# Optimization experiments

Hardware: AMD Instinct MI355X
Metric: run time of the kernel (lower is better)

Reference implementation:

```python
import jax, jax.numpy as jnp
import numpy as np

N_NODES = 50000


def _sage_conv(x, src, dst, W_l, b_l, W_r):
    # mean aggregation of source-node features at destination nodes
    msg_sum = jax.ops.segment_sum(x[src], dst, num_segments=N_NODES)  # [N, d_in]
    deg = jax.ops.segment_sum(jnp.ones((src.shape[0],), x.dtype), dst,
                              num_segments=N_NODES)  # [N]
    mean = msg_sum / jnp.maximum(deg, 1.0)[:, None]
    # SAGEConv: lin_l(aggr) + lin_r(x); lin_l has bias, lin_r does not
    return mean @ W_l + b_l + x @ W_r


def setup_inputs() -> dict:
    key = jax.random.key(0)
    ks = jax.random.split(key, 8)
    d_in, d_hid, d_out = 128, 128, 64
    E = 800000
    s = lambda k, shp: jax.random.normal(k, shp, dtype=jnp.float32) * (1.0 / np.sqrt(shp[0]))
    return {
        "x": jax.random.normal(ks[0], (N_NODES, d_in), dtype=jnp.float32),
        "edge_index": jax.random.randint(ks[1], (2, E), 0, N_NODES, dtype=jnp.int64
                                         if jax.config.jax_enable_x64 else jnp.int32),
        "W_l1": s(ks[2], (d_in, d_hid)),
        "b_l1": jnp.zeros((d_hid,), jnp.float32),
        "W_r1": s(ks[3], (d_in, d_hid)),
        "W_l2": s(ks[4], (d_hid, d_out)),
        "b_l2": jnp.zeros((d_out,), jnp.float32),
        "W_r2": s(ks[5], (d_hid, d_out)),
    }


def reference(x, edge_index, W_l1, b_l1, W_r1, W_l2, b_l2, W_r2):
    src, dst = edge_index[0], edge_index[1]
    h = _sage_conv(x, src, dst, W_l1, b_l1, W_r1)
    h = jax.nn.relu(h)  # dropout is identity in eval mode
    h = _sage_conv(h, src, dst, W_l2, b_l2, W_r2)
    return h
```

## Files before the change

### kernel.cpp

```cpp
#include <hip/hip_runtime.h>
#include <hip/hip_bf16.h>

#define N_NODES 50000
#define M_TILES 3125
#define NBUCKET 196
#define CAP 5120
#define CHUNK_A 3125
#define CONV_BLOCKS 6250

typedef __attribute__((ext_vector_type(8))) __bf16 bf16x8;
typedef __attribute__((ext_vector_type(4))) float f32x4;

#define OFF_OFF   0
#define OFFE_OFF  200192
#define EBUF_OFF  400384
#define GCUR_OFF  2407424
#define INV_OFF   3800576
#define XBF_OFF   4000768
#define AGG_OFF   16800768
#define PAIRS_OFF 29600768
#define PBF_OFF   42400768
#define WP1_OFF   48800768
#define WP2_OFF   48866304

__device__ __forceinline__ unsigned bfbits(float f) {
    unsigned u = __float_as_uint(f);
    return (u + 0x7fffu + ((u >> 16) & 1u)) & 0xffff0000u;
}
__device__ __forceinline__ unsigned short bf16r(float f) {
    return (unsigned short)(bfbits(f) >> 16);
}
__device__ __forceinline__ float blo(unsigned u) { return __uint_as_float(u << 16); }
__device__ __forceinline__ float bhi(unsigned u) { return __uint_as_float(u & 0xffff0000u); }

__global__ __launch_bounds__(256) void prep_kernel(const float4* __restrict__ x4,
                                                   uint2* __restrict__ xbf,
                                                   int* __restrict__ gcur,
                                                   const float* __restrict__ Wl1,
                                                   const float* __restrict__ Wr1,
                                                   const float* __restrict__ Wl2,
                                                   const float* __restrict__ Wr2,
                                                   unsigned short* __restrict__ Wp1,
                                                   unsigned short* __restrict__ Wp2) {
    int bid = blockIdx.x;
    int t = threadIdx.x;
    if (bid < CONV_BLOCKS) {
        if (bid == 0 && t < NBUCKET) gcur[t] = 0;
        int i = bid * 256 + t;
        float4 v = x4[i];
        uint2 o;
        o.x = (bfbits(v.x) >> 16) | bfbits(v.y);
        o.y = (bfbits(v.z) >> 16) | bfbits(v.w);
        xbf[i] = o;
    } else if (bid < CONV_BLOCKS + 128) {
        int idx = (bid - CONV_BLOCKS) * 256 + t;
        int k = idx >> 7, n = idx & 127;
        float v = (k < 128) ? Wl1[k * 128 + n] : Wr1[(k - 128) * 128 + n];
        Wp1[((k >> 5) << 12) + (n << 5) + (((k >> 3) & 3) << 3) + (k & 7)] = bf16r(v);
    } else {
        int idx = (bid - CONV_BLOCKS - 128) * 256 + t;
        int k = idx >> 7, n = idx & 127;
        float v = (n < 64) ? Wl2[k * 64 + n] : Wr2[k * 64 + (n - 64)];
        Wp2[((k >> 5) << 12) + (n << 5) + (((k >> 3) & 3) << 3) + (k & 7)] = bf16r(v);
    }
}

__global__ __launch_bounds__(256) void passA_kernel(const int* __restrict__ src,
                                                    const int* __restrict__ dst,
                                                    int* __restrict__ gcur,
                                                    unsigned* __restrict__ pairs, int E) {
    __shared__ int bh[256];
    __shared__ int lcur[256];
    __shared__ int gb[256];
    __shared__ int sc[256];
    __shared__ unsigned lbuf[3328];
    int t = threadIdx.x;
    int e0 = blockIdx.x * CHUNK_A;
    int e1 = min(e0 + CHUNK_A, E);
    bh[t] = 0;
    lcur[t] = 0;
    __syncthreads();
    for (int e = e0 + t; e < e1; e += 256) atomicAdd(&bh[dst[e] >> 8], 1);
    __syncthreads();
    int v = bh[t];
    sc[t] = v;
    __syncthreads();
    for (int d = 1; d < 256; d <<= 1) {
        int u = (t >= d) ? sc[t - d] : 0;
        __syncthreads();
        sc[t] += u;
        __syncthreads();
    }
    int lbase = sc[t] - v;
    if (v > 0) gb[t] = t * CAP + atomicAdd(&gcur[t], v);
    bh[t] = lbase;
    __syncthreads();
    for (int e = e0 + t; e < e1; e += 256) {
        int s = src[e], d = dst[e];
        int b = d >> 8;
        int lpos = bh[b] + atomicAdd(&lcur[b], 1);
        lbuf[lpos] = (unsigned)s | ((unsigned)d << 16);
    }
    __syncthreads();
    int T = e1 - e0;
    for (int k = t; k < T; k += 256) {
        unsigned p = lbuf[k];
        int b = p >> 24;
        pairs[gb[b] + (k - bh[b])] = p;
    }
}

__global__ __launch_bounds__(256) void passB_kernel(const int* __restrict__ gcur,
                                                    const unsigned* __restrict__ pairs,
                                                    int* __restrict__ off,
                                                    int* __restrict__ offE,
                                                    float* __restrict__ invdeg,
                                                    unsigned short* __restrict__ ebuf16) {
    __shared__ int sc[256];
    __shared__ int fh[256];
    __shared__ int lcnt[256];
    __shared__ unsigned short lout[CAP];
    int b = blockIdx.x;
    int t = threadIdx.x;
    int gb = b * CAP;
    int W = gcur[b];
    fh[t] = 0;
    __syncthreads();
    for (int k = t; k < W; k += 256) atomicAdd(&fh[(pairs[gb + k] >> 16) & 255], 1);
    __syncthreads();
    int c = fh[t];
    sc[t] = c;
    __syncthreads();
    for (int d = 1; d < 256; d <<= 1) {
        int u = (t >= d) ? sc[t - d] : 0;
        __syncthreads();
        sc[t] += u;
        __syncthreads();
    }
    int excl = sc[t] - c;
    int dg = b * 256 + t;
    if (dg < N_NODES) {
        off[dg] = gb + excl;
        offE[dg] = gb + excl + c;
        invdeg[dg] = 1.0f / fmaxf((float)c, 1.0f);
    }
    lcnt[t] = excl;
    __syncthreads();
    for (int k = t; k < W; k += 256) {
        unsigned p = pairs[gb + k];
        int dl = (p >> 16) & 255;
        int pos = atomicAdd(&lcnt[dl], 1);
        lout[pos] = (unsigned short)(p & 0xffffu);
    }
    __syncthreads();
    for (int k = t; k < W; k += 256) ebuf16[gb + k] = lout[k];
}

__global__ __launch_bounds__(64) void gather1_kernel(const int* __restrict__ off,
                                                     const int* __restrict__ offE,
                                                     const unsigned short* __restrict__ ebuf,
                                                     const float* __restrict__ invdeg,
                                                     const uint4* __restrict__ xbf4,
                                                     uint4* __restrict__ aggbf4) {
    int d = blockIdx.x;
    int j = threadIdx.x;
    int g = j >> 4;
    int f = j & 15;
    int lo = off[d], hi = offE[d];
    float a[8] = {0.f, 0.f, 0.f, 0.f, 0.f, 0.f, 0.f, 0.f};
    int i = lo + g;
    for (; i + 12 < hi; i += 16) {
        int s0 = ebuf[i], s1 = ebuf[i + 4], s2 = ebuf[i + 8], s3 = ebuf[i + 12];
        uint4 v0 = xbf4[(size_t)s0 * 16 + f];
        uint4 v1 = xbf4[(size_t)s1 * 16 + f];
        uint4 v2 = xbf4[(size_t)s2 * 16 + f];
        uint4 v3 = xbf4[(size_t)s3 * 16 + f];
        a[0] += blo(v0.x) + blo(v1.x) + blo(v2.x) + blo(v3.x);
        a[1] += bhi(v0.x) + bhi(v1.x) + bhi(v2.x) + bhi(v3.x);
        a[2] += blo(v0.y) + blo(v1.y) + blo(v2.y) + blo(v3.y);
        a[3] += bhi(v0.y) + bhi(v1.y) + bhi(v2.y) + bhi(v3.y);
        a[4] += blo(v0.z) + blo(v1.z) + blo(v2.z) + blo(v3.z);
        a[5] += bhi(v0.z) + bhi(v1.z) + bhi(v2.z) + bhi(v3.z);
        a[6] += blo(v0.w) + blo(v1.w) + blo(v2.w) + blo(v3.w);
        a[7] += bhi(v0.w) + bhi(v1.w) + bhi(v2.w) + bhi(v3.w);
    }
    for (; i < hi; i += 4) {
        uint4 v = xbf4[(size_t)ebuf[i] * 16 + f];
        a[0] += blo(v.x); a[1] += bhi(v.x);
        a[2] += blo(v.y); a[3] += bhi(v.y);
        a[4] += blo(v.z); a[5] += bhi(v.z);
        a[6] += blo(v.w); a[7] += bhi(v.w);
    }
#pragma unroll
    for (int q = 0; q < 8; ++q) {
        a[q] += __shfl_xor(a[q], 16, 64);
        a[q] += __shfl_xor(a[q], 32, 64);
    }
    if (g == 0) {
        float inv = invdeg[d];
        uint4 o;
        o.x = (bfbits(a[0] * inv) >> 16) | bfbits(a[1] * inv);
        o.y = (bfbits(a[2] * inv) >> 16) | bfbits(a[3] * inv);
        o.z = (bfbits(a[4] * inv) >> 16) | bfbits(a[5] * inv);
        o.w = (bfbits(a[6] * inv) >> 16) | bfbits(a[7] * inv);
        aggbf4[(size_t)d * 16 + f] = o;
    }
}

__global__ __launch_bounds__(256) void gemmF_kernel(const unsigned short* __restrict__ aggbf,
                                                    const unsigned short* __restrict__ xbf,
                                                    const unsigned short* __restrict__ Wp1,
                                                    const float* __restrict__ b1,
                                                    const unsigned short* __restrict__ Wp2,
                                                    const float* __restrict__ b2,
                                                    unsigned short* __restrict__ pbf,
                                                    float* __restrict__ out) {
    __shared__ unsigned short hsm[4][2][2048];
    int w = threadIdx.x >> 6;
    int pairIdx = blockIdx.x * 4 + w;
    int tile0 = pairIdx * 2;
    int tile1 = tile0 + 1;
    bool act0 = tile0 < M_TILES;
    bool act1 = tile1 < M_TILES;
    int t0 = act0 ? tile0 : 0;
    int t1 = act1 ? tile1 : 0;
    int lane = threadIdx.x & 63;
    int lo16 = lane & 15;
    int kg = lane >> 4;
    int r0 = kg * 4;

    f32x4 accA[8], accB[8];
#pragma unroll
    for (int n = 0; n < 8; ++n) {
        accA[n] = (f32x4){0.f, 0.f, 0.f, 0.f};
        accB[n] = (f32x4){0.f, 0.f, 0.f, 0.f};
    }
    const unsigned short* rowa0 = aggbf + (size_t)(t0 * 16 + lo16) * 128;
    const unsigned short* rowx0 = xbf + (size_t)(t0 * 16 + lo16) * 128;
    const unsigned short* rowa1 = aggbf + (size_t)(t1 * 16 + lo16) * 128;
    const unsigned short* rowx1 = xbf + (size_t)(t1 * 16 + lo16) * 128;
#pragma unroll
    for (int ks = 0; ks < 8; ++ks) {
        int ao = (ks < 4 ? ks * 32 : (ks - 4) * 32) + kg * 8;
        bf16x8 a0 = *reinterpret_cast<const bf16x8*>((ks < 4 ? rowa0 : rowx0) + ao);
        bf16x8 a1 = *reinterpret_cast<const bf16x8*>((ks < 4 ? rowa1 : rowx1) + ao);
        const unsigned short* wbase = Wp1 + ks * 4096 + lo16 * 32 + kg * 8;
#pragma unroll
        for (int n = 0; n < 8; ++n) {
            bf16x8 b = *reinterpret_cast<const bf16x8*>(wbase + n * 512);
            accA[n] = __builtin_amdgcn_mfma_f32_16x16x32_bf16(a0, b, accA[n], 0, 0, 0);
            accB[n] = __builtin_amdgcn_mfma_f32_16x16x32_bf16(a1, b, accB[n], 0, 0, 0);
        }
    }

    unsigned short* hs0 = hsm[w][0];
    unsigned short* hs1 = hsm[w][1];
#pragma unroll
    for (int n = 0; n < 8; ++n) {
        int col = n * 16 + lo16;
        float bv = b1[col];
#pragma unroll
        for (int r = 0; r < 4; ++r) {
            int row = r0 + r;
            int sw = (col ^ ((row & 7) << 3));
            hs0[row * 128 + sw] = bf16r(fmaxf(accA[n][r] + bv, 0.0f));
            hs1[row * 128 + sw] = bf16r(fmaxf(accB[n][r] + bv, 0.0f));
        }
    }
    __syncthreads();

    f32x4 acc2A[8], acc2B[8];
#pragma unroll
    for (int n = 0; n < 8; ++n) {
        acc2A[n] = (f32x4){0.f, 0.f, 0.f, 0.f};
        acc2B[n] = (f32x4){0.f, 0.f, 0.f, 0.f};
    }
#pragma unroll
    for (int ks = 0; ks < 4; ++ks) {
        int base0 = (ks * 32 + kg * 8) ^ ((lo16 & 7) << 3);
        bf16x8 a20 = *reinterpret_cast<const bf16x8*>(&hs0[lo16 * 128 + base0]);
        bf16x8 a21 = *reinterpret_cast<const bf16x8*>(&hs1[lo16 * 128 + base0]);
        const unsigned short* wbase = Wp2 + ks * 4096 + lo16 * 32 + kg * 8;
#pragma unroll
        for (int n = 0; n < 8; ++n) {
            bf16x8 b = *reinterpret_cast<const bf16x8*>(wbase + n * 512);
            acc2A[n] = __builtin_amdgcn_mfma_f32_16x16x32_bf16(a20, b, acc2A[n], 0, 0, 0);
            acc2B[n] = __builtin_amdgcn_mfma_f32_16x16x32_bf16(a21, b, acc2B[n], 0, 0, 0);
        }
    }

#pragma unroll
    for (int n = 0; n < 8; ++n) {
        int col = n * 16 + lo16;
        if (col < 64) {
#pragma unroll
            for (int r = 0; r < 4; ++r) {
                if (act0) pbf[(size_t)(tile0 * 16 + r0 + r) * 64 + col] = bf16r(acc2A[n][r]);
                if (act1) pbf[(size_t)(tile1 * 16 + r0 + r) * 64 + col] = bf16r(acc2B[n][r]);
            }
        } else {
            float bv = b2[col - 64];
#pragma unroll
            for (int r = 0; r < 4; ++r) {
                if (act0) out[(size_t)(tile0 * 16 + r0 + r) * 64 + (col - 64)] = acc2A[n][r] + bv;
                if (act1) out[(size_t)(tile1 * 16 + r0 + r) * 64 + (col - 64)] = acc2B[n][r] + bv;
            }
        }
    }
}

__global__ __launch_bounds__(64) void gather2_kernel(const int* __restrict__ off,
                                                     const int* __restrict__ offE,
                                                     const unsigned short* __restrict__ ebuf,
                                                     const float* __restrict__ invdeg,
                                                     const uint2* __restrict__ pbf2,
                                                     float4* __restrict__ out4) {
    int d = blockIdx.x;
    int j = threadIdx.x;
    int g = j >> 4;
    int f = j & 15;
    int lo = off[d], hi = offE[d];
    float a0 = 0.f, a1 = 0.f, a2 = 0.f, a3 = 0.f;
    int i = lo + g;
    for (; i + 12 < hi; i += 16) {
        int s0 = ebuf[i], s1 = ebuf[i + 4], s2 = ebuf[i + 8], s3 = ebuf[i + 12];
        uint2 v0 = pbf2[(size_t)s0 * 16 + f];
        uint2 v1 = pbf2[(size_t)s1 * 16 + f];
        uint2 v2 = pbf2[(size_t)s2 * 16 + f];
        uint2 v3 = pbf2[(size_t)s3 * 16 + f];
        a0 += blo(v0.x) + blo(v1.x) + blo(v2.x) + blo(v3.x);
        a1 += bhi(v0.x) + bhi(v1.x) + bhi(v2.x) + bhi(v3.x);
        a2 += blo(v0.y) + blo(v1.y) + blo(v2.y) + blo(v3.y);
        a3 += bhi(v0.y) + bhi(v1.y) + bhi(v2.y) + bhi(v3.y);
    }
    for (; i < hi; i += 4) {
        uint2 v = pbf2[(size_t)ebuf[i] * 16 + f];
        a0 += blo(v.x); a1 += bhi(v.x);
        a2 += blo(v.y); a3 += bhi(v.y);
    }
    a0 += __shfl_xor(a0, 16, 64); a0 += __shfl_xor(a0, 32, 64);
    a1 += __shfl_xor(a1, 16, 64); a1 += __shfl_xor(a1, 32, 64);
    a2 += __shfl_xor(a2, 16, 64); a2 += __shfl_xor(a2, 32, 64);
    a3 += __shfl_xor(a3, 16, 64); a3 += __shfl_xor(a3, 32, 64);
    if (g == 0) {
        float inv = invdeg[d];
        float4* op = out4 + (size_t)d * 16 + f;
        float4 o = *op;
        o.x += a0 * inv;
        o.y += a1 * inv;
        o.z += a2 * inv;
        o.w += a3 * inv;
        *op = o;
    }
}

extern "C" void kernel_launch(void* const* d_in, const int* in_sizes, int n_in,
                              void* d_out, int out_size, void* d_ws, size_t ws_size,
                              hipStream_t stream) {
    const float* x   = (const float*)d_in[0];
    const int*   ei  = (const int*)d_in[1];
    const float* Wl1 = (const float*)d_in[2];
    const float* b1  = (const float*)d_in[3];
    const float* Wr1 = (const float*)d_in[4];
    const float* Wl2 = (const float*)d_in[5];
    const float* b2  = (const float*)d_in[6];
    const float* Wr2 = (const float*)d_in[7];
    float* out = (float*)d_out;

    const int E = in_sizes[1] / 2;
    const int* src = ei;
    const int* dst = ei + E;

    char* ws = (char*)d_ws;
    int*            off    = (int*)(ws + OFF_OFF);
    int*            offE   = (int*)(ws + OFFE_OFF);
    unsigned short* ebuf16 = (unsigned short*)(ws + EBUF_OFF);
    int*            gcur   = (int*)(ws + GCUR_OFF);
    float*          invdeg = (float*)(ws + INV_OFF);
    unsigned*       xbf    = (unsigned*)(ws + XBF_OFF);
    unsigned*       aggbf  = (unsigned*)(ws + AGG_OFF);
    unsigned*       pairs  = (unsigned*)(ws + PAIRS_OFF);
    unsigned short* pbf    = (unsigned short*)(ws + PBF_OFF);
    unsigned short* Wp1    = (unsigned short*)(ws + WP1_OFF);
    unsigned short* Wp2    = (unsigned short*)(ws + WP2_OFF);

    prep_kernel<<<CONV_BLOCKS + 192, 256, 0, stream>>>((const float4*)x, (uint2*)xbf, gcur,
                                                       Wl1, Wr1, Wl2, Wr2, Wp1, Wp2);

    passA_kernel<<<(E + CHUNK_A - 1) / CHUNK_A, 256, 0, stream>>>(src, dst, gcur, pairs, E);
    passB_kernel<<<NBUCKET, 256, 0, stream>>>(gcur, pairs, off, offE, invdeg, ebuf16);

    gather1_kernel<<<N_NODES, 64, 0, stream>>>(off, offE, ebuf16, invdeg, (const uint4*)xbf,
                                               (uint4*)aggbf);

    gemmF_kernel<<<(((M_TILES + 1) / 2) + 3) / 4, 256, 0, stream>>>(
        (const unsigned short*)aggbf, (const unsigned short*)xbf,
        Wp1, b1, Wp2, b2, pbf, out);

    gather2_kernel<<<N_NODES, 64, 0, stream>>>(off, offE, ebuf16, invdeg, (const uint2*)pbf,
                                               (float4*)out);
}
```

Baseline: 112.4 us.

## Fuse layer-1 gather into GEMM kernel and merge prep with bucketing pass

The first-layer neighbour gather is folded into the fused GEMM kernel. Each wave aggregates its own 16-node tile, with 4 lanes per node, into swizzled LDS, so the bf16 aggregate buffer is no longer written to and read back from global memory. The conversion/prep kernel and passA are merged into one launch, and gcur is zeroed with a memset. The cost is a less parallel gather: one wave per 16 nodes, serial over edges per lane with many registers, which may reduce memory-level parallelism and occupancy compared with the per-node 64-thread gather. GEMM tile pairing per wave is also dropped.

```diff
diff --git a/kernel.cpp b/kernel.cpp
--- a/kernel.cpp
+++ b/kernel.cpp
@@ -17,7 +17,6 @@
 #define GCUR_OFF  2407424
 #define INV_OFF   3800576
 #define XBF_OFF   4000768
-#define AGG_OFF   16800768
 #define PAIRS_OFF 29600768
 #define PBF_OFF   42400768
 #define WP1_OFF   48800768
@@ -33,39 +32,15 @@
 __device__ __forceinline__ float blo(unsigned u) { return __uint_as_float(u << 16); }
 __device__ __forceinline__ float bhi(unsigned u) { return __uint_as_float(u & 0xffff0000u); }
 
-__global__ __launch_bounds__(256) void prep_kernel(const float4* __restrict__ x4,
-                                                   uint2* __restrict__ xbf,
-                                                   int* __restrict__ gcur,
-                                                   const float* __restrict__ Wl1,
-                                                   const float* __restrict__ Wr1,
-                                                   const float* __restrict__ Wl2,
-                                                   const float* __restrict__ Wr2,
-                                                   unsigned short* __restrict__ Wp1,
-                                                   unsigned short* __restrict__ Wp2) {
-    int bid = blockIdx.x;
-    int t = threadIdx.x;
-    if (bid < CONV_BLOCKS) {
-        if (bid == 0 && t < NBUCKET) gcur[t] = 0;
-        int i = bid * 256 + t;
-        float4 v = x4[i];
-        uint2 o;
-        o.x = (bfbits(v.x) >> 16) | bfbits(v.y);
-        o.y = (bfbits(v.z) >> 16) | bfbits(v.w);
-        xbf[i] = o;
-    } else if (bid < CONV_BLOCKS + 128) {
-        int idx = (bid - CONV_BLOCKS) * 256 + t;
-        int k = idx >> 7, n = idx & 127;
-        float v = (k < 128) ? Wl1[k * 128 + n] : Wr1[(k - 128) * 128 + n];
-        Wp1[((k >> 5) << 12) + (n << 5) + (((k >> 3) & 3) << 3) + (k & 7)] = bf16r(v);
-    } else {
-        int idx = (bid - CONV_BLOCKS - 128) * 256 + t;
-        int k = idx >> 7, n = idx & 127;
-        float v = (n < 64) ? Wl2[k * 64 + n] : Wr2[k * 64 + (n - 64)];
-        Wp2[((k >> 5) << 12) + (n << 5) + (((k >> 3) & 3) << 3) + (k & 7)] = bf16r(v);
-    }
-}
-
-__global__ __launch_bounds__(256) void passA_kernel(const int* __restrict__ src,
+__global__ __launch_bounds__(256) void prepA_kernel(const float4* __restrict__ x4,
+                                                    uint2* __restrict__ xbf,
+                                                    const float* __restrict__ Wl1,
+                                                    const float* __restrict__ Wr1,
+                                                    const float* __restrict__ Wl2,
+                                                    const float* __restrict__ Wr2,
+                                                    unsigned short* __restrict__ Wp1,
+                                                    unsigned short* __restrict__ Wp2,
+                                                    const int* __restrict__ src,
                                                     const int* __restrict__ dst,
                                                     int* __restrict__ gcur,
                                                     unsigned* __restrict__ pairs, int E) {
@@ -74,8 +49,35 @@
     __shared__ int gb[256];
     __shared__ int sc[256];
     __shared__ unsigned lbuf[3328];
+    int bid = blockIdx.x;
     int t = threadIdx.x;
-    int e0 = blockIdx.x * CHUNK_A;
+    if (bid < CONV_BLOCKS) {
+        int i = bid * 256 + t;
+        float4 v = x4[i];
+        uint2 o;
+        o.x = (bfbits(v.x) >> 16) | bfbits(v.y);
+        o.y = (bfbits(v.z) >> 16) | bfbits(v.w);
+        xbf[i] = o;
+        return;
+    }
+    bid -= CONV_BLOCKS;
+    if (bid < 128) {
+        int idx = bid * 256 + t;
+        int k = idx >> 7, n = idx & 127;
+        float v = (k < 128) ? Wl1[k * 128 + n] : Wr1[(k - 128) * 128 + n];
+        Wp1[((k >> 5) << 12) + (n << 5) + (((k >> 3) & 3) << 3) + (k & 7)] = bf16r(v);
+        return;
+    }
+    bid -= 128;
+    if (bid < 64) {
+        int idx = bid * 256 + t;
+        int k = idx >> 7, n = idx & 127;
+        float v = (n < 64) ? Wl2[k * 64 + n] : Wr2[k * 64 + (n - 64)];
+        Wp2[((k >> 5) << 12) + (n << 5) + (((k >> 3) & 3) << 3) + (k & 7)] = bf16r(v);
+        return;
+    }
+    bid -= 64;
+    int e0 = bid * CHUNK_A;
     int e1 = min(e0 + CHUNK_A, E);
     bh[t] = 0;
     lcur[t] = 0;
@@ -156,58 +158,11 @@
     for (int k = t; k < W; k += 256) ebuf16[gb + k] = lout[k];
 }
 
-__global__ __launch_bounds__(64) void gather1_kernel(const int* __restrict__ off,
-                                                     const int* __restrict__ offE,
-                                                     const unsigned short* __restrict__ ebuf,
-                                                     const float* __restrict__ invdeg,
-                                                     const uint4* __restrict__ xbf4,
-                                                     uint4* __restrict__ aggbf4) {
-    int d = blockIdx.x;
-    int j = threadIdx.x;
-    int g = j >> 4;
-    int f = j & 15;
-    int lo = off[d], hi = offE[d];
-    float a[8] = {0.f, 0.f, 0.f, 0.f, 0.f, 0.f, 0.f, 0.f};
-    int i = lo + g;
-    for (; i + 12 < hi; i += 16) {
-        int s0 = ebuf[i], s1 = ebuf[i + 4], s2 = ebuf[i + 8], s3 = ebuf[i + 12];
-        uint4 v0 = xbf4[(size_t)s0 * 16 + f];
-        uint4 v1 = xbf4[(size_t)s1 * 16 + f];
-        uint4 v2 = xbf4[(size_t)s2 * 16 + f];
-        uint4 v3 = xbf4[(size_t)s3 * 16 + f];
-        a[0] += blo(v0.x) + blo(v1.x) + blo(v2.x) + blo(v3.x);
-        a[1] += bhi(v0.x) + bhi(v1.x) + bhi(v2.x) + bhi(v3.x);
-        a[2] += blo(v0.y) + blo(v1.y) + blo(v2.y) + blo(v3.y);
-        a[3] += bhi(v0.y) + bhi(v1.y) + bhi(v2.y) + bhi(v3.y);
-        a[4] += blo(v0.z) + blo(v1.z) + blo(v2.z) + blo(v3.z);
-        a[5] += bhi(v0.z) + bhi(v1.z) + bhi(v2.z) + bhi(v3.z);
-        a[6] += blo(v0.w) + blo(v1.w) + blo(v2.w) + blo(v3.w);
-        a[7] += bhi(v0.w) + bhi(v1.w) + bhi(v2.w) + bhi(v3.w);
-    }
-    for (; i < hi; i += 4) {
-        uint4 v = xbf4[(size_t)ebuf[i] * 16 + f];
-        a[0] += blo(v.x); a[1] += bhi(v.x);
-        a[2] += blo(v.y); a[3] += bhi(v.y);
-        a[4] += blo(v.z); a[5] += bhi(v.z);
-        a[6] += blo(v.w); a[7] += bhi(v.w);
-    }
-#pragma unroll
-    for (int q = 0; q < 8; ++q) {
-        a[q] += __shfl_xor(a[q], 16, 64);
-        a[q] += __shfl_xor(a[q], 32, 64);
-    }
-    if (g == 0) {
-        float inv = invdeg[d];
-        uint4 o;
-        o.x = (bfbits(a[0] * inv) >> 16) | bfbits(a[1] * inv);
-        o.y = (bfbits(a[2] * inv) >> 16) | bfbits(a[3] * inv);
-        o.z = (bfbits(a[4] * inv) >> 16) | bfbits(a[5] * inv);
-        o.w = (bfbits(a[6] * inv) >> 16) | bfbits(a[7] * inv);
-        aggbf4[(size_t)d * 16 + f] = o;
-    }
-}
-
-__global__ __launch_bounds__(256) void gemmF_kernel(const unsigned short* __restrict__ aggbf,
+__global__ __launch_bounds__(256) void fuse1_kernel(const int* __restrict__ off,
+                                                    const int* __restrict__ offE,
+                                                    const unsigned short* __restrict__ ebuf,
+                                                    const float* __restrict__ invdeg,
+                                                    const uint4* __restrict__ xbf4,
                                                     const unsigned short* __restrict__ xbf,
                                                     const unsigned short* __restrict__ Wp1,
                                                     const float* __restrict__ b1,
@@ -215,46 +170,88 @@
                                                     const float* __restrict__ b2,
                                                     unsigned short* __restrict__ pbf,
                                                     float* __restrict__ out) {
-    __shared__ unsigned short hsm[4][2][2048];
+    __shared__ unsigned short lsm[4][2048];
     int w = threadIdx.x >> 6;
-    int pairIdx = blockIdx.x * 4 + w;
-    int tile0 = pairIdx * 2;
-    int tile1 = tile0 + 1;
-    bool act0 = tile0 < M_TILES;
-    bool act1 = tile1 < M_TILES;
-    int t0 = act0 ? tile0 : 0;
-    int t1 = act1 ? tile1 : 0;
+    int tile = blockIdx.x * 4 + w;
+    if (tile >= M_TILES) return;
     int lane = threadIdx.x & 63;
+    unsigned short* ls = lsm[w];
+
+    int node = tile * 16 + (lane >> 2);
+    int q = lane & 3;
+    int lo = off[node], hi = offE[node];
+    float a[4][8];
+#pragma unroll
+    for (int u = 0; u < 4; ++u)
+#pragma unroll
+        for (int j = 0; j < 8; ++j) a[u][j] = 0.f;
+    int i = lo;
+    for (; i + 1 < hi; i += 2) {
+        int s0 = ebuf[i], s1 = ebuf[i + 1];
+        uint4 v0[4], v1[4];
+#pragma unroll
+        for (int u = 0; u < 4; ++u) v0[u] = xbf4[(size_t)s0 * 16 + q * 4 + u];
+#pragma unroll
+        for (int u = 0; u < 4; ++u) v1[u] = xbf4[(size_t)s1 * 16 + q * 4 + u];
+#pragma unroll
+        for (int u = 0; u < 4; ++u) {
+            a[u][0] += blo(v0[u].x) + blo(v1[u].x); a[u][1] += bhi(v0[u].x) + bhi(v1[u].x);
+            a[u][2] += blo(v0[u].y) + blo(v1[u].y); a[u][3] += bhi(v0[u].y) + bhi(v1[u].y);
+            a[u][4] += blo(v0[u].z) + blo(v1[u].z); a[u][5] += bhi(v0[u].z) + bhi(v1[u].z);
+            a[u][6] += blo(v0[u].w) + blo(v1[u].w); a[u][7] += bhi(v0[u].w) + bhi(v1[u].w);
+        }
+    }
+    if (i < hi) {
+        int s0 = ebuf[i];
+#pragma unroll
+        for (int u = 0; u < 4; ++u) {
+            uint4 v = xbf4[(size_t)s0 * 16 + q * 4 + u];
+            a[u][0] += blo(v.x); a[u][1] += bhi(v.x);
+            a[u][2] += blo(v.y); a[u][3] += bhi(v.y);
+            a[u][4] += blo(v.z); a[u][5] += bhi(v.z);
+            a[u][6] += blo(v.w); a[u][7] += bhi(v.w);
+        }
+    }
+    {
+        float inv = invdeg[node];
+        int row = lane >> 2;
+        int sx = (row & 7) << 3;
+#pragma unroll
+        for (int u = 0; u < 4; ++u) {
+#pragma unroll
+            for (int j = 0; j < 4; ++j) {
+                unsigned pk = (bfbits(a[u][2 * j] * inv) >> 16) | bfbits(a[u][2 * j + 1] * inv);
+                int col = q * 32 + u * 8 + 2 * j;
+                *reinterpret_cast<unsigned*>(&ls[row * 128 + (col ^ sx)]) = pk;
+            }
+        }
+    }
+
     int lo16 = lane & 15;
     int kg = lane >> 4;
+    int m0 = tile * 16;
     int r0 = kg * 4;
-
-    f32x4 accA[8], accB[8];
-#pragma unroll
-    for (int n = 0; n < 8; ++n) {
-        accA[n] = (f32x4){0.f, 0.f, 0.f, 0.f};
-        accB[n] = (f32x4){0.f, 0.f, 0.f, 0.f};
-    }
-    const unsigned short* rowa0 = aggbf + (size_t)(t0 * 16 + lo16) * 128;
-    const unsigned short* rowx0 = xbf + (size_t)(t0 * 16 + lo16) * 128;
-    const unsigned short* rowa1 = aggbf + (size_t)(t1 * 16 + lo16) * 128;
-    const unsigned short* rowx1 = xbf + (size_t)(t1 * 16 + lo16) * 128;
+    int asw = (lo16 & 7) << 3;
+
+    f32x4 acc[8];
+#pragma unroll
+    for (int n = 0; n < 8; ++n) acc[n] = (f32x4){0.f, 0.f, 0.f, 0.f};
+    const unsigned short* rowx = xbf + (size_t)(m0 + lo16) * 128;
 #pragma unroll
     for (int ks = 0; ks < 8; ++ks) {
-        int ao = (ks < 4 ? ks * 32 : (ks - 4) * 32) + kg * 8;
-        bf16x8 a0 = *reinterpret_cast<const bf16x8*>((ks < 4 ? rowa0 : rowx0) + ao);
-        bf16x8 a1 = *reinterpret_cast<const bf16x8*>((ks < 4 ? rowa1 : rowx1) + ao);
+        bf16x8 aF;
+        if (ks < 4)
+            aF = *reinterpret_cast<const bf16x8*>(&ls[lo16 * 128 + ((ks * 32 + kg * 8) ^ asw)]);
+        else
+            aF = *reinterpret_cast<const bf16x8*>(rowx + (ks - 4) * 32 + kg * 8);
         const unsigned short* wbase = Wp1 + ks * 4096 + lo16 * 32 + kg * 8;
 #pragma unroll
         for (int n = 0; n < 8; ++n) {
             bf16x8 b = *reinterpret_cast<const bf16x8*>(wbase + n * 512);
-            accA[n] = __builtin_amdgcn_mfma_f32_16x16x32_bf16(a0, b, accA[n], 0, 0, 0);
-            accB[n] = __builtin_amdgcn_mfma_f32_16x16x32_bf16(a1, b, accB[n], 0, 0, 0);
-        }
-    }
-
-    unsigned short* hs0 = hsm[w][0];
-    unsigned short* hs1 = hsm[w][1];
+            acc[n] = __builtin_amdgcn_mfma_f32_16x16x32_bf16(aF, b, acc[n], 0, 0, 0);
+        }
+    }
+
 #pragma unroll
     for (int n = 0; n < 8; ++n) {
         int col = n * 16 + lo16;
@@ -262,30 +259,21 @@
 #pragma unroll
         for (int r = 0; r < 4; ++r) {
             int row = r0 + r;
-            int sw = (col ^ ((row & 7) << 3));
-            hs0[row * 128 + sw] = bf16r(fmaxf(accA[n][r] + bv, 0.0f));
-            hs1[row * 128 + sw] = bf16r(fmaxf(accB[n][r] + bv, 0.0f));
-        }
-    }
-    __syncthreads();
-
-    f32x4 acc2A[8], acc2B[8];
-#pragma unroll
-    for (int n = 0; n < 8; ++n) {
-        acc2A[n] = (f32x4){0.f, 0.f, 0.f, 0.f};
-        acc2B[n] = (f32x4){0.f, 0.f, 0.f, 0.f};
-    }
+            ls[row * 128 + (col ^ ((row & 7) << 3))] = bf16r(fmaxf(acc[n][r] + bv, 0.0f));
+        }
+    }
+
+    f32x4 acc2[8];
+#pragma unroll
+    for (int n = 0; n < 8; ++n) acc2[n] = (f32x4){0.f, 0.f, 0.f, 0.f};
 #pragma unroll
     for (int ks = 0; ks < 4; ++ks) {
-        int base0 = (ks * 32 + kg * 8) ^ ((lo16 & 7) << 3);
-        bf16x8 a20 = *reinterpret_cast<const bf16x8*>(&hs0[lo16 * 128 + base0]);
-        bf16x8 a21 = *reinterpret_cast<const bf16x8*>(&hs1[lo16 * 128 + base0]);
+        bf16x8 a2 = *reinterpret_cast<const bf16x8*>(&ls[lo16 * 128 + ((ks * 32 + kg * 8) ^ asw)]);
         const unsigned short* wbase = Wp2 + ks * 4096 + lo16 * 32 + kg * 8;
 #pragma unroll
         for (int n = 0; n < 8; ++n) {
             bf16x8 b = *reinterpret_cast<const bf16x8*>(wbase + n * 512);
-            acc2A[n] = __builtin_amdgcn_mfma_f32_16x16x32_bf16(a20, b, acc2A[n], 0, 0, 0);
-            acc2B[n] = __builtin_amdgcn_mfma_f32_16x16x32_bf16(a21, b, acc2B[n], 0, 0, 0);
+            acc2[n] = __builtin_amdgcn_mfma_f32_16x16x32_bf16(a2, b, acc2[n], 0, 0, 0);
         }
     }
 
@@ -294,17 +282,13 @@
         int col = n * 16 + lo16;
         if (col < 64) {
 #pragma unroll
-            for (int r = 0; r < 4; ++r) {
-                if (act0) pbf[(size_t)(tile0 * 16 + r0 + r) * 64 + col] = bf16r(acc2A[n][r]);
-                if (act1) pbf[(size_t)(tile1 * 16 + r0 + r) * 64 + col] = bf16r(acc2B[n][r]);
-            }
+            for (int r = 0; r < 4; ++r)
+                pbf[(size_t)(m0 + r0 + r) * 64 + col] = bf16r(acc2[n][r]);
         } else {
             float bv = b2[col - 64];
 #pragma unroll
-            for (int r = 0; r < 4; ++r) {
-                if (act0) out[(size_t)(tile0 * 16 + r0 + r) * 64 + (col - 64)] = acc2A[n][r] + bv;
-                if (act1) out[(size_t)(tile1 * 16 + r0 + r) * 64 + (col - 64)] = acc2B[n][r] + bv;
-            }
+            for (int r = 0; r < 4; ++r)
+                out[(size_t)(m0 + r0 + r) * 64 + (col - 64)] = acc2[n][r] + bv;
         }
     }
 }
@@ -378,23 +362,21 @@
     int*            gcur   = (int*)(ws + GCUR_OFF);
     float*          invdeg = (float*)(ws + INV_OFF);
     unsigned*       xbf    = (unsigned*)(ws + XBF_OFF);
-    unsigned*       aggbf  = (unsigned*)(ws + AGG_OFF);
     unsigned*       pairs  = (unsigned*)(ws + PAIRS_OFF);
     unsigned short* pbf    = (unsigned short*)(ws + PBF_OFF);
     unsigned short* Wp1    = (unsigned short*)(ws + WP1_OFF);
     unsigned short* Wp2    = (unsigned short*)(ws + WP2_OFF);
 
-    prep_kernel<<<CONV_BLOCKS + 192, 256, 0, stream>>>((const float4*)x, (uint2*)xbf, gcur,
-                                                       Wl1, Wr1, Wl2, Wr2, Wp1, Wp2);
-
-    passA_kernel<<<(E + CHUNK_A - 1) / CHUNK_A, 256, 0, stream>>>(src, dst, gcur, pairs, E);
+    (void)hipMemsetAsync(gcur, 0, NBUCKET * sizeof(int), stream);
+
+    prepA_kernel<<<CONV_BLOCKS + 192 + 256, 256, 0, stream>>>(
+        (const float4*)x, (uint2*)xbf, Wl1, Wr1, Wl2, Wr2, Wp1, Wp2,
+        src, dst, gcur, pairs, E);
+
     passB_kernel<<<NBUCKET, 256, 0, stream>>>(gcur, pairs, off, offE, invdeg, ebuf16);
 
-    gather1_kernel<<<N_NODES, 64, 0, stream>>>(off, offE, ebuf16, invdeg, (const uint4*)xbf,
-                                               (uint4*)aggbf);
-
-    gemmF_kernel<<<(((M_TILES + 1) / 2) + 3) / 4, 256, 0, stream>>>(
-        (const unsigned short*)aggbf, (const unsigned short*)xbf,
+    fuse1_kernel<<<(M_TILES + 3) / 4, 256, 0, stream>>>(
+        off, offE, ebuf16, invdeg, (const uint4*)xbf, (const unsigned short*)xbf,
         Wp1, b1, Wp2, b2, pbf, out);
 
     gather2_kernel<<<N_NODES, 64, 0, stream>>>(off, offE, ebuf16, invdeg, (const uint2*)pbf,
```

Measured after the change: 121.7 us. 8.4% more time.
